# Kernel tuning notes

Hardware: AMD Instinct MI355X
Metric: run time of the kernel (lower is better)

## Reference

```python
import jax, jax.numpy as jnp
import numpy as np

B, T_Q, T_C = 4, 2048, 2048
Q_DIM = C_DIM = H_DIM = OUT_DIM = 1024
N_HEADS = 16
D = H_DIM // N_HEADS


def setup_inputs() -> dict:
    key = jax.random.key(0)
    ks = jax.random.split(key, 10)
    s_q = 1.0 / np.sqrt(Q_DIM)
    s_c = 1.0 / np.sqrt(C_DIM)
    s_h = 1.0 / np.sqrt(H_DIM)
    return {
        "query": jax.random.normal(ks[0], (B, T_Q, Q_DIM), jnp.float32),
        "context": jax.random.normal(ks[1], (B, T_C, C_DIM), jnp.float32),
        "Wq": jax.random.uniform(ks[2], (Q_DIM, H_DIM), jnp.float32, -s_q, s_q),
        "bq": jax.random.uniform(ks[3], (H_DIM,), jnp.float32, -s_q, s_q),
        "Wk": jax.random.uniform(ks[4], (C_DIM, H_DIM), jnp.float32, -s_c, s_c),
        "bk": jax.random.uniform(ks[5], (H_DIM,), jnp.float32, -s_c, s_c),
        "Wv": jax.random.uniform(ks[6], (C_DIM, H_DIM), jnp.float32, -s_c, s_c),
        "bv": jax.random.uniform(ks[7], (H_DIM,), jnp.float32, -s_c, s_c),
        "Wo": jax.random.uniform(ks[8], (H_DIM, OUT_DIM), jnp.float32, -s_h, s_h),
        "bo": jax.random.uniform(ks[9], (OUT_DIM,), jnp.float32, -s_h, s_h),
    }


def reference(query, context, Wq, bq, Wk, bk, Wv, bv, Wo, bo):
    Bq, Tq, _ = query.shape
    _, Tc, _ = context.shape
    # project and split heads: [B, H, T, D]
    q = (query @ Wq + bq).reshape(Bq, Tq, N_HEADS, D).transpose(0, 2, 1, 3)
    k = (context @ Wk + bk).reshape(Bq, Tc, N_HEADS, D).transpose(0, 2, 1, 3)
    v = (context @ Wv + bv).reshape(Bq, Tc, N_HEADS, D).transpose(0, 2, 1, 3)
    scores = jnp.einsum("bhqd,bhkd->bhqk", q, k) / jnp.sqrt(jnp.float32(D))
    probs = jax.nn.softmax(scores, axis=-1)
    attn = jnp.einsum("bhqk,bhkd->bhqd", probs, v)  # dropout p=0 -> identity
    attn = attn.transpose(0, 2, 1, 3).reshape(Bq, Tq, N_HEADS * D)
    return attn @ Wo + bo
```

## Files before the change

kernel.cpp:

```cpp
#include <hip/hip_runtime.h>
#include <hip/hip_bf16.h>
#include <cstdint>

typedef __attribute__((ext_vector_type(8))) short short8;
typedef __attribute__((ext_vector_type(4))) short short4_t;
typedef __attribute__((ext_vector_type(4))) float f32x4;

#define MFMA16(a, b, c) __builtin_amdgcn_mfma_f32_16x16x32_bf16(a, b, c, 0, 0, 0)

__device__ __forceinline__ short f2b(float f) {
    union { float fp; unsigned u; } un; un.fp = f;
    unsigned r = un.u + 0x7fffu + ((un.u >> 16) & 1u);
    return (short)(r >> 16);
}

#if __has_builtin(__builtin_amdgcn_cvt_pk_bf16_f32)
__device__ __forceinline__ unsigned pk_bf16(float a, float b) {
    auto r = __builtin_amdgcn_cvt_pk_bf16_f32(a, b);
    unsigned u; __builtin_memcpy(&u, &r, 4); return u;
}
#else
__device__ __forceinline__ unsigned pk_bf16(float a, float b) {
    return (unsigned)(unsigned short)f2b(a) | ((unsigned)(unsigned short)f2b(b) << 16);
}
#endif

typedef const __attribute__((address_space(1))) unsigned g_as1;
typedef __attribute__((address_space(3))) unsigned l_as3;
__device__ __forceinline__ void gll16(const ushort* g, ushort* l) {
    __builtin_amdgcn_global_load_lds((g_as1*)g, (l_as3*)l, 16, 0, 0);
}

__global__ __launch_bounds__(256) void in_cvt_kernel(
    const float* __restrict__ q, const float* __restrict__ c,
    ushort* __restrict__ qb, ushort* __restrict__ cb)
{
    const float* src = blockIdx.y ? c : q;
    ushort* dst = blockIdx.y ? cb : qb;
    size_t i = ((size_t)blockIdx.x * 256 + threadIdx.x) * 8;
    float4 v0 = *(const float4*)&src[i];
    float4 v1 = *(const float4*)&src[i + 4];
    uint4 o;
    o.x = pk_bf16(v0.x, v0.y); o.y = pk_bf16(v0.z, v0.w);
    o.z = pk_bf16(v1.x, v1.y); o.w = pk_bf16(v1.z, v1.w);
    *(uint4*)&dst[i] = o;
}

__global__ __launch_bounds__(256) void wt_cvt_kernel(
    const float* __restrict__ Wq, const float* __restrict__ Wk,
    const float* __restrict__ Wv, const float* __restrict__ Wo,
    ushort* __restrict__ wt)
{
    __shared__ float Ts[64 * 65];
    const int z = blockIdx.z;
    const float* W = (z == 0) ? Wq : (z == 1) ? Wk : (z == 2) ? Wv : Wo;
    ushort* WT = wt + (size_t)z * (1024 * 1024);
    const int n0 = blockIdx.x * 64, k0 = blockIdx.y * 64;
    const int tid = threadIdx.x;

#pragma unroll
    for (int rr = 0; rr < 4; ++rr) {
        int u = tid + rr * 256;
        int r = u >> 4, c = (u & 15) * 4;
        float4 v = *(const float4*)&W[(size_t)(k0 + r) * 1024 + n0 + c];
        Ts[r * 65 + c + 0] = v.x; Ts[r * 65 + c + 1] = v.y;
        Ts[r * 65 + c + 2] = v.z; Ts[r * 65 + c + 3] = v.w;
    }
    __syncthreads();
#pragma unroll
    for (int rr = 0; rr < 4; ++rr) {
        int u = tid + rr * 256;
        int rn = u >> 4, ck = (u & 15) * 4;
        short4_t o;
        o[0] = f2b(Ts[(ck + 0) * 65 + rn]);
        o[1] = f2b(Ts[(ck + 1) * 65 + rn]);
        o[2] = f2b(Ts[(ck + 2) * 65 + rn]);
        o[3] = f2b(Ts[(ck + 3) * 65 + rn]);
        *(short4_t*)&WT[(size_t)(n0 + rn) * 1024 + k0 + ck] = o;
    }
}

template <int MODE>
__global__ __launch_bounds__(256) void gemm_kernel(
    const ushort* __restrict__ Ag, const ushort* __restrict__ BT,
    const float* __restrict__ bias, void* __restrict__ Outp, float scale)
{
    __shared__ ushort As[128 * 64];
    __shared__ ushort Bs[128 * 64];
    const int tid = threadIdx.x;
    const int w = tid >> 6, lane = tid & 63;
    const int ln = tid & 15, quad = (tid >> 4) & 3;
    const int wm = w >> 1, wn = w & 1;
    const int m0 = blockIdx.y * 128, n0 = blockIdx.x * 128;

    int offA[4], offB[4], lseg[4];
#pragma unroll
    for (int rr = 0; rr < 4; ++rr) {
        int idx = (rr * 4 + w) * 64 + lane;
        int r = idx >> 3, cst = idx & 7, csrc = cst ^ (r & 7);
        offA[rr] = (m0 + r) * 1024 + csrc * 8;
        offB[rr] = (n0 + r) * 1024 + csrc * 8;
        lseg[rr] = (rr * 4 + w) * 512;
    }

    f32x4 acc[4][4] = {};

    for (int kk = 0; kk < 1024; kk += 64) {
        __syncthreads();
#pragma unroll
        for (int rr = 0; rr < 4; ++rr)
            gll16(&Ag[(size_t)(offA[rr] + kk)], &As[lseg[rr]]);
#pragma unroll
        for (int rr = 0; rr < 4; ++rr)
            gll16(&BT[(size_t)(offB[rr] + kk)], &Bs[lseg[rr]]);
        __syncthreads();

#pragma unroll
        for (int ks = 0; ks < 2; ++ks) {
            short8 af[4], bfr[4];
#pragma unroll
            for (int i = 0; i < 4; ++i)
                af[i] = *(const short8*)&As[(wm * 64 + i * 16 + ln) * 64 +
                                            ((ks * 4 + quad) ^ (ln & 7)) * 8];
#pragma unroll
            for (int j = 0; j < 4; ++j)
                bfr[j] = *(const short8*)&Bs[(wn * 64 + j * 16 + ln) * 64 +
                                             ((ks * 4 + quad) ^ (ln & 7)) * 8];
#pragma unroll
            for (int i = 0; i < 4; ++i)
#pragma unroll
                for (int j = 0; j < 4; ++j)
                    acc[i][j] = MFMA16(af[i], bfr[j], acc[i][j]);
        }
    }

#pragma unroll
    for (int j = 0; j < 4; ++j) {
        int n = n0 + wn * 64 + j * 16 + ln;
        float bv = bias[n];
#pragma unroll
        for (int i = 0; i < 4; ++i) {
            int mb = m0 + wm * 64 + i * 16 + quad * 4;
            if (MODE == 3) {
                float* Out = (float*)Outp;
#pragma unroll
                for (int r = 0; r < 4; ++r)
                    Out[(size_t)(mb + r) * 1024 + n] = acc[i][j][r] + bv;
            } else {
                ushort* Out = (ushort*)Outp;
                int h = n >> 6, d = n & 63;
#pragma unroll
                for (int r = 0; r < 4; ++r) {
                    int m = mb + r, b = m >> 11, t = m & 2047;
                    Out[(((size_t)(b * 16 + h) * 2048 + t) << 6) + d] =
                        (ushort)f2b((acc[i][j][r] + bv) * scale);
                }
            }
        }
    }
}

__global__ __launch_bounds__(256) void kv_kernel(
    const ushort* __restrict__ Cb, const ushort* __restrict__ WTk,
    const ushort* __restrict__ WTv,
    const float* __restrict__ bk, const float* __restrict__ bv,
    ushort* __restrict__ Kw, ushort* __restrict__ Vtw)
{
    __shared__ ushort As[128 * 64];
    __shared__ ushort Bs[128 * 64];
    const int tid = threadIdx.x;
    const int w = tid >> 6, lane = tid & 63;
    const int ln = tid & 15, quad = (tid >> 4) & 3;
    const int wm = w >> 1, wn = w & 1;
    const int z = blockIdx.x >> 3;
    const int n0 = (blockIdx.x & 7) * 128;
    const int m0 = blockIdx.y * 128;
    const ushort* BT = z ? WTv : WTk;

    int offA[4], offB[4], lseg[4];
#pragma unroll
    for (int rr = 0; rr < 4; ++rr) {
        int idx = (rr * 4 + w) * 64 + lane;
        int r = idx >> 3, cst = idx & 7, csrc = cst ^ (r & 7);
        offA[rr] = (m0 + r) * 1024 + csrc * 8;
        offB[rr] = (n0 + r) * 1024 + csrc * 8;
        lseg[rr] = (rr * 4 + w) * 512;
    }

    f32x4 acc[4][4] = {};

    for (int kk = 0; kk < 1024; kk += 64) {
        __syncthreads();
#pragma unroll
        for (int rr = 0; rr < 4; ++rr)
            gll16(&Cb[(size_t)(offA[rr] + kk)], &As[lseg[rr]]);
#pragma unroll
        for (int rr = 0; rr < 4; ++rr)
            gll16(&BT[(size_t)(offB[rr] + kk)], &Bs[lseg[rr]]);
        __syncthreads();

#pragma unroll
        for (int ks = 0; ks < 2; ++ks) {
            short8 af[4], bfr[4];
#pragma unroll
            for (int i = 0; i < 4; ++i)
                af[i] = *(const short8*)&As[(wm * 64 + i * 16 + ln) * 64 +
                                            ((ks * 4 + quad) ^ (ln & 7)) * 8];
#pragma unroll
            for (int j = 0; j < 4; ++j)
                bfr[j] = *(const short8*)&Bs[(wn * 64 + j * 16 + ln) * 64 +
                                             ((ks * 4 + quad) ^ (ln & 7)) * 8];
#pragma unroll
            for (int i = 0; i < 4; ++i)
#pragma unroll
                for (int j = 0; j < 4; ++j)
                    acc[i][j] = MFMA16(af[i], bfr[j], acc[i][j]);
        }
    }

#pragma unroll
    for (int j = 0; j < 4; ++j) {
        int n = n0 + wn * 64 + j * 16 + ln;
        int h = n >> 6, d = n & 63;
        if (z == 0) {
            float bvv = bk[n];
#pragma unroll
            for (int i = 0; i < 4; ++i) {
                int mb = m0 + wm * 64 + i * 16 + quad * 4;
#pragma unroll
                for (int r = 0; r < 4; ++r) {
                    int m = mb + r, b = m >> 11, t = m & 2047;
                    Kw[(((size_t)(b * 16 + h) * 2048 + t) << 6) + d] =
                        (ushort)f2b(acc[i][j][r] + bvv);
                }
            }
        } else {
            float bvv = bv[n];
#pragma unroll
            for (int i = 0; i < 4; ++i) {
                int mb = m0 + wm * 64 + i * 16 + quad * 4;
                int b = mb >> 11, t = mb & 2047;
                short4_t o;
                o[0] = f2b(acc[i][j][0] + bvv); o[1] = f2b(acc[i][j][1] + bvv);
                o[2] = f2b(acc[i][j][2] + bvv); o[3] = f2b(acc[i][j][3] + bvv);
                *(short4_t*)&Vtw[(((size_t)((b * 16 + h) * 64 + d)) << 11) + t] = o;
            }
        }
    }
}

__global__ __launch_bounds__(256, 3) void attn_kernel(
    const ushort* __restrict__ Qw, const ushort* __restrict__ Kw,
    const ushort* __restrict__ Vtw, ushort* __restrict__ attn)
{
    __shared__ ushort Ks[2 * 4096];
    __shared__ ushort Vts[2 * 4096];
    __shared__ ushort Ps[128 * 64];
    __shared__ float red[128];

    const int tid = threadIdx.x;
    const int w = tid >> 6, lane = tid & 63;
    const int ln = tid & 15, quad = (tid >> 4) & 3;
    const int bh = blockIdx.y, b = bh >> 4, h = bh & 15;
    const int qt = blockIdx.x;

    const ushort* Qg = Qw + (size_t)bh * 131072 + (size_t)qt * 8192;
    const ushort* Kg = Kw + (size_t)bh * 131072;
    const ushort* Vg = Vtw + (size_t)bh * 131072;

    short8 bq[2][2];
#pragma unroll
    for (int qs = 0; qs < 2; ++qs)
#pragma unroll
        for (int ks = 0; ks < 2; ++ks)
            bq[qs][ks] = *(const short8*)&Qg[(w * 32 + qs * 16 + ln) * 64 + ks * 32 + quad * 8];

    int offK[2], offV[2], lseg[2];
#pragma unroll
    for (int rr = 0; rr < 2; ++rr) {
        int idx = (rr * 4 + w) * 64 + lane;
        int r = idx >> 3, cst = idx & 7, csrc = cst ^ (r & 7);
        offK[rr] = r * 64 + csrc * 8;
        offV[rr] = r * 2048 + csrc * 8;
        lseg[rr] = (rr * 4 + w) * 512;
    }

#pragma unroll
    for (int rr = 0; rr < 2; ++rr) gll16(&Kg[offK[rr]], &Ks[lseg[rr]]);
#pragma unroll
    for (int rr = 0; rr < 2; ++rr) gll16(&Vg[offV[rr]], &Vts[lseg[rr]]);

    f32x4 Of[2][4] = {};
    float psum[2] = {0.f, 0.f};

    for (int kt = 0; kt < 32; ++kt) {
        __syncthreads();
        const int cur = (kt & 1) * 4096;
        if (kt < 31) {
            const int nx = 4096 - cur;
#pragma unroll
            for (int rr = 0; rr < 2; ++rr)
                gll16(&Kg[(kt + 1) * 4096 + offK[rr]], &Ks[nx + lseg[rr]]);
#pragma unroll
            for (int rr = 0; rr < 2; ++rr)
                gll16(&Vg[(kt + 1) * 64 + offV[rr]], &Vts[nx + lseg[rr]]);
        }
        const ushort* ksm = &Ks[cur];
        const ushort* vsm = &Vts[cur];

        f32x4 sa[4][2];
#pragma unroll
        for (int kv = 0; kv < 4; ++kv) {
            short8 a0 = *(const short8*)&ksm[(kv * 16 + ln) * 64 + (quad ^ (ln & 7)) * 8];
            short8 a1 = *(const short8*)&ksm[(kv * 16 + ln) * 64 + ((4 + quad) ^ (ln & 7)) * 8];
#pragma unroll
            for (int qs = 0; qs < 2; ++qs) {
                f32x4 s = {};
                s = MFMA16(a0, bq[qs][0], s);
                s = MFMA16(a1, bq[qs][1], s);
                sa[kv][qs] = s;
            }
        }

#pragma unroll
        for (int qs = 0; qs < 2; ++qs) {
            int qrow = w * 32 + qs * 16 + ln;
#pragma unroll
            for (int kv = 0; kv < 4; ++kv) {
                float p0 = __builtin_amdgcn_exp2f(sa[kv][qs][0]);
                float p1 = __builtin_amdgcn_exp2f(sa[kv][qs][1]);
                float p2 = __builtin_amdgcn_exp2f(sa[kv][qs][2]);
                float p3 = __builtin_amdgcn_exp2f(sa[kv][qs][3]);
                psum[qs] += (p0 + p1) + (p2 + p3);
                uint2 pk2;
                pk2.x = pk_bf16(p0, p1);
                pk2.y = pk_bf16(p2, p3);
                int c = 2 * kv + (quad >> 1);
                *(uint2*)&Ps[qrow * 64 + ((c ^ (ln & 7)) * 8) + (quad & 1) * 4] = pk2;
            }
        }

#pragma unroll
        for (int ks = 0; ks < 2; ++ks) {
            short8 vb[4], pa[2];
#pragma unroll
            for (int ds = 0; ds < 4; ++ds)
                vb[ds] = *(const short8*)&vsm[(ds * 16 + ln) * 64 +
                                              ((ks * 4 + quad) ^ (ln & 7)) * 8];
#pragma unroll
            for (int qs = 0; qs < 2; ++qs)
                pa[qs] = *(const short8*)&Ps[(w * 32 + qs * 16 + ln) * 64 +
                                             ((ks * 4 + quad) ^ (ln & 7)) * 8];
#pragma unroll
            for (int qs = 0; qs < 2; ++qs)
#pragma unroll
                for (int ds = 0; ds < 4; ++ds)
                    Of[qs][ds] = MFMA16(pa[qs], vb[ds], Of[qs][ds]);
        }
    }

#pragma unroll
    for (int qs = 0; qs < 2; ++qs) {
        float l = psum[qs];
        l += __shfl_xor(l, 16);
        l += __shfl_xor(l, 32);
        if (quad == 0) red[w * 32 + qs * 16 + ln] = __builtin_amdgcn_rcpf(l);
    }
    __syncthreads();

#pragma unroll
    for (int qs = 0; qs < 2; ++qs) {
        f32x4 inv = *(const f32x4*)&red[w * 32 + qs * 16 + quad * 4];
#pragma unroll
        for (int ds = 0; ds < 4; ++ds) {
#pragma unroll
            for (int r = 0; r < 4; ++r) {
                int t = qt * 128 + w * 32 + qs * 16 + quad * 4 + r;
                int col = h * 64 + ds * 16 + ln;
                attn[((size_t)(b * 2048 + t) << 10) + col] =
                    (ushort)f2b(Of[qs][ds][r] * inv[r]);
            }
        }
    }
}

extern "C" void kernel_launch(void* const* d_in, const int* in_sizes, int n_in,
                              void* d_out, int out_size, void* d_ws, size_t ws_size,
                              hipStream_t stream)
{
    const float* query   = (const float*)d_in[0];
    const float* context = (const float*)d_in[1];
    const float* Wq = (const float*)d_in[2];
    const float* bq = (const float*)d_in[3];
    const float* Wk = (const float*)d_in[4];
    const float* bk = (const float*)d_in[5];
    const float* Wv = (const float*)d_in[6];
    const float* bv = (const float*)d_in[7];
    const float* Wo = (const float*)d_in[8];
    const float* bo = (const float*)d_in[9];

    char* ws = (char*)d_ws;
    ushort* WT  = (ushort*)ws;
    ushort* Qb  = (ushort*)(ws + 8388608);
    ushort* Qw  = (ushort*)(ws + 25165824);
    ushort* Kw  = (ushort*)(ws + 41943040);
    ushort* Vtw = (ushort*)(ws + 58720256);
    ushort* Aw  = Qb;
    ushort* Cb  = (ushort*)d_out;

    const float SCALE = 0.18033688011112042f;

    in_cvt_kernel<<<dim3(4096, 2), 256, 0, stream>>>(query, context, Qb, Cb);
    wt_cvt_kernel<<<dim3(16, 16, 4), 256, 0, stream>>>(Wq, Wk, Wv, Wo, WT);
    gemm_kernel<0><<<dim3(8, 64), 256, 0, stream>>>(Qb, WT + 0 * 1048576, bq, Qw, SCALE);
    kv_kernel<<<dim3(16, 64), 256, 0, stream>>>(Cb, WT + 1 * 1048576,
                                                WT + 2 * 1048576, bk, bv, Kw, Vtw);
    attn_kernel<<<dim3(16, 64), 256, 0, stream>>>(Qw, Kw, Vtw, Aw);
    gemm_kernel<3><<<dim3(8, 64), 256, 0, stream>>>(Aw, WT + 3 * 1048576, bo,
                                                    (float*)d_out, 1.0f);
}
```

Before: 329.3 us.

## Keep attention probabilities in registers via K16 MFMA, drop LDS P staging

Reworks the attention kernel so the exponentiated scores stay in registers and feed 16x16x16 MFMAs directly as the B operand, removing the LDS round-trip for P. The row sums are computed with an MFMA against a vector of ones instead of shuffles and a shared reduction. The double-buffered K/V prefetch is replaced by a single buffer loaded synchronously each iteration, and occupancy is raised to 4 blocks per SM; the output store is vectorised to packed 64-bit writes. The trade-off is losing load/compute overlap and using half-rate K16 MFMAs for the PV product.

```diff
diff --git a/kernel.cpp b/kernel.cpp
--- a/kernel.cpp
+++ b/kernel.cpp
@@ -7,6 +7,7 @@
 typedef __attribute__((ext_vector_type(4))) float f32x4;
 
 #define MFMA16(a, b, c) __builtin_amdgcn_mfma_f32_16x16x32_bf16(a, b, c, 0, 0, 0)
+#define MFMA16K16(a, b, c) __builtin_amdgcn_mfma_f32_16x16x16bf16_1k(a, b, c, 0, 0, 0)
 
 __device__ __forceinline__ short f2b(float f) {
     union { float fp; unsigned u; } un; un.fp = f;
@@ -24,6 +25,8 @@
     return (unsigned)(unsigned short)f2b(a) | ((unsigned)(unsigned short)f2b(b) << 16);
 }
 #endif
+
+union pk4_u { unsigned u2[2]; short4_t s; };
 
 typedef const __attribute__((address_space(1))) unsigned g_as1;
 typedef __attribute__((address_space(3))) unsigned l_as3;
@@ -249,14 +252,12 @@
     }
 }
 
-__global__ __launch_bounds__(256, 3) void attn_kernel(
+__global__ __launch_bounds__(256, 4) void attn_kernel(
     const ushort* __restrict__ Qw, const ushort* __restrict__ Kw,
     const ushort* __restrict__ Vtw, ushort* __restrict__ attn)
 {
-    __shared__ ushort Ks[2 * 4096];
-    __shared__ ushort Vts[2 * 4096];
-    __shared__ ushort Ps[128 * 64];
-    __shared__ float red[128];
+    __shared__ ushort Ks[4096];
+    __shared__ ushort Vts[4096];
 
     const int tid = threadIdx.x;
     const int w = tid >> 6, lane = tid & 63;
@@ -285,34 +286,26 @@
         lseg[rr] = (rr * 4 + w) * 512;
     }
 
-#pragma unroll
-    for (int rr = 0; rr < 2; ++rr) gll16(&Kg[offK[rr]], &Ks[lseg[rr]]);
-#pragma unroll
-    for (int rr = 0; rr < 2; ++rr) gll16(&Vg[offV[rr]], &Vts[lseg[rr]]);
+    const short4_t ones = {(short)0x3F80, (short)0x3F80, (short)0x3F80, (short)0x3F80};
 
     f32x4 Of[2][4] = {};
-    float psum[2] = {0.f, 0.f};
+    f32x4 lac[2] = {};
 
     for (int kt = 0; kt < 32; ++kt) {
         __syncthreads();
-        const int cur = (kt & 1) * 4096;
-        if (kt < 31) {
-            const int nx = 4096 - cur;
-#pragma unroll
-            for (int rr = 0; rr < 2; ++rr)
-                gll16(&Kg[(kt + 1) * 4096 + offK[rr]], &Ks[nx + lseg[rr]]);
-#pragma unroll
-            for (int rr = 0; rr < 2; ++rr)
-                gll16(&Vg[(kt + 1) * 64 + offV[rr]], &Vts[nx + lseg[rr]]);
-        }
-        const ushort* ksm = &Ks[cur];
-        const ushort* vsm = &Vts[cur];
+#pragma unroll
+        for (int rr = 0; rr < 2; ++rr)
+            gll16(&Kg[kt * 4096 + offK[rr]], &Ks[lseg[rr]]);
+#pragma unroll
+        for (int rr = 0; rr < 2; ++rr)
+            gll16(&Vg[kt * 64 + offV[rr]], &Vts[lseg[rr]]);
+        __syncthreads();
 
         f32x4 sa[4][2];
 #pragma unroll
         for (int kv = 0; kv < 4; ++kv) {
-            short8 a0 = *(const short8*)&ksm[(kv * 16 + ln) * 64 + (quad ^ (ln & 7)) * 8];
-            short8 a1 = *(const short8*)&ksm[(kv * 16 + ln) * 64 + ((4 + quad) ^ (ln & 7)) * 8];
+            short8 a0 = *(const short8*)&Ks[(kv * 16 + ln) * 64 + (quad ^ (ln & 7)) * 8];
+            short8 a1 = *(const short8*)&Ks[(kv * 16 + ln) * 64 + ((4 + quad) ^ (ln & 7)) * 8];
 #pragma unroll
             for (int qs = 0; qs < 2; ++qs) {
                 f32x4 s = {};
@@ -322,64 +315,46 @@
             }
         }
 
-#pragma unroll
-        for (int qs = 0; qs < 2; ++qs) {
-            int qrow = w * 32 + qs * 16 + ln;
+        short4_t pf[4][2];
+#pragma unroll
+        for (int qs = 0; qs < 2; ++qs)
 #pragma unroll
             for (int kv = 0; kv < 4; ++kv) {
                 float p0 = __builtin_amdgcn_exp2f(sa[kv][qs][0]);
                 float p1 = __builtin_amdgcn_exp2f(sa[kv][qs][1]);
                 float p2 = __builtin_amdgcn_exp2f(sa[kv][qs][2]);
                 float p3 = __builtin_amdgcn_exp2f(sa[kv][qs][3]);
-                psum[qs] += (p0 + p1) + (p2 + p3);
-                uint2 pk2;
-                pk2.x = pk_bf16(p0, p1);
-                pk2.y = pk_bf16(p2, p3);
-                int c = 2 * kv + (quad >> 1);
-                *(uint2*)&Ps[qrow * 64 + ((c ^ (ln & 7)) * 8) + (quad & 1) * 4] = pk2;
-            }
-        }
-
-#pragma unroll
-        for (int ks = 0; ks < 2; ++ks) {
-            short8 vb[4], pa[2];
-#pragma unroll
-            for (int ds = 0; ds < 4; ++ds)
-                vb[ds] = *(const short8*)&vsm[(ds * 16 + ln) * 64 +
-                                              ((ks * 4 + quad) ^ (ln & 7)) * 8];
-#pragma unroll
-            for (int qs = 0; qs < 2; ++qs)
-                pa[qs] = *(const short8*)&Ps[(w * 32 + qs * 16 + ln) * 64 +
-                                             ((ks * 4 + quad) ^ (ln & 7)) * 8];
-#pragma unroll
-            for (int qs = 0; qs < 2; ++qs)
-#pragma unroll
-                for (int ds = 0; ds < 4; ++ds)
-                    Of[qs][ds] = MFMA16(pa[qs], vb[ds], Of[qs][ds]);
+                pk4_u pu;
+                pu.u2[0] = pk_bf16(p0, p1);
+                pu.u2[1] = pk_bf16(p2, p3);
+                pf[kv][qs] = pu.s;
+                lac[qs] = MFMA16K16(ones, pu.s, lac[qs]);
+            }
+
+#pragma unroll
+        for (int kv = 0; kv < 4; ++kv) {
+#pragma unroll
+            for (int ds = 0; ds < 4; ++ds) {
+                short4_t vf = *(const short4_t*)&Vts[(ds * 16 + ln) * 64 +
+                    (((2 * kv + (quad >> 1)) ^ (ln & 7)) * 8) + (quad & 1) * 4];
+#pragma unroll
+                for (int qs = 0; qs < 2; ++qs)
+                    Of[qs][ds] = MFMA16K16(vf, pf[kv][qs], Of[qs][ds]);
+            }
         }
     }
 
 #pragma unroll
     for (int qs = 0; qs < 2; ++qs) {
-        float l = psum[qs];
-        l += __shfl_xor(l, 16);
-        l += __shfl_xor(l, 32);
-        if (quad == 0) red[w * 32 + qs * 16 + ln] = __builtin_amdgcn_rcpf(l);
-    }
-    __syncthreads();
-
-#pragma unroll
-    for (int qs = 0; qs < 2; ++qs) {
-        f32x4 inv = *(const f32x4*)&red[w * 32 + qs * 16 + quad * 4];
+        float inv = __builtin_amdgcn_rcpf(lac[qs][0]);
+        int t = qt * 128 + w * 32 + qs * 16 + ln;
+        size_t base = ((size_t)(b * 2048 + t) << 10) + h * 64;
 #pragma unroll
         for (int ds = 0; ds < 4; ++ds) {
-#pragma unroll
-            for (int r = 0; r < 4; ++r) {
-                int t = qt * 128 + w * 32 + qs * 16 + quad * 4 + r;
-                int col = h * 64 + ds * 16 + ln;
-                attn[((size_t)(b * 2048 + t) << 10) + col] =
-                    (ushort)f2b(Of[qs][ds][r] * inv[r]);
-            }
+            uint2 o;
+            o.x = pk_bf16(Of[qs][ds][0] * inv, Of[qs][ds][1] * inv);
+            o.y = pk_bf16(Of[qs][ds][2] * inv, Of[qs][ds][3] * inv);
+            *(uint2*)&attn[base + ds * 16 + quad * 4] = o;
         }
     }
 }
```

Result: no change. 326.1 us (-1.0%).
